# Kernel optimization log

Measured on AMD Instinct MI355X. Metric: run time of the kernel, lower is better.

Reference implementation:

```python
import jax, jax.numpy as jnp
import numpy as np

MAX_CH = 21
LAT_DIM = 64
D_EMBED = 1024
N_HEADS = 16
D_HEAD = D_EMBED // N_HEADS  # 64
L = MAX_CH * LAT_DIM         # 1344 latents
B, T = 4, 1024


def setup_inputs() -> dict:
    key = jax.random.key(0)
    k1, k2, k3, k4, k5, k6 = jax.random.split(key, 6)
    x = jax.random.normal(k1, (B, T, D_EMBED), dtype=jnp.float32)
    # boolean channel mask [b, L, T]
    ch_mask = jax.random.randint(k2, (B, L, T), 0, 2) > 0
    # learned latent queries [L, H*d] (xavier-uniform-ish init)
    lim_q = float(np.sqrt(6.0 / (L + N_HEADS * D_HEAD)))
    latent_q = jax.random.uniform(k3, (L, N_HEADS * D_HEAD), minval=-lim_q, maxval=lim_q, dtype=jnp.float32)
    # Linear weights (torch layout: [out, in]) and biases
    lim_w = float(np.sqrt(1.0 / D_EMBED))
    w_k_w = jax.random.uniform(k4, (N_HEADS * D_HEAD, D_EMBED), minval=-lim_w, maxval=lim_w, dtype=jnp.float32)
    w_k_b = jnp.zeros((N_HEADS * D_HEAD,), dtype=jnp.float32)
    w_v_w = jax.random.uniform(k5, (N_HEADS * D_HEAD, D_EMBED), minval=-lim_w, maxval=lim_w, dtype=jnp.float32)
    w_v_b = jax.random.uniform(k6, (N_HEADS * D_HEAD,), minval=-lim_w, maxval=lim_w, dtype=jnp.float32)
    return {"x": x, "ch_mask": ch_mask, "latent_q": latent_q,
            "w_k_w": w_k_w, "w_k_b": w_k_b, "w_v_w": w_v_w, "w_v_b": w_v_b}


def reference(x, ch_mask, latent_q, w_k_w, w_k_b, w_v_w, w_v_b):
    b, t, d = x.shape
    H, dh = N_HEADS, D_HEAD
    l = latent_q.shape[0]
    # faithful to torch .view(-1, H, L, d): raw row-major reinterpretation
    lq = latent_q.reshape(1, H, l, dh)                    # [1,H,L,dh]
    k = (x @ w_k_w.T + w_k_b).reshape(b, t, H, dh).transpose(0, 2, 3, 1)  # [b,H,dh,T]
    v = (x @ w_v_w.T + w_v_b).reshape(b, t, H, dh).transpose(0, 2, 1, 3)  # [b,H,T,dh]
    scale = jnp.float32(H) ** -0.5  # note: n_heads**-0.5, as in source
    scores = jnp.einsum('ohld,bhdt->bhlt', lq, k) * scale  # [b,H,L,T]
    mask = ch_mask[:, None, :, :]                           # [b,1,L,T] broadcast over heads
    scores = jnp.where(mask, scores, jnp.float32(-1e9))
    w = jax.nn.softmax(scores, axis=-1)
    w = jnp.where(mask, w, jnp.float32(0.0))
    out = jnp.einsum('bhlt,bhtd->bhld', w, v)               # [b,H,L,dh]
    return out.transpose(0, 2, 1, 3).reshape(b, l, H * dh)  # [b,L,H*dh]
```

## Files before the change

kernel.cpp:

```cpp
#include <hip/hip_runtime.h>
#include <hip/hip_bf16.h>

#define B_SZ 4
#define T_SZ 1024
#define NH 16
#define L_SZ 1344
#define LT_COUNT 21

typedef __attribute__((ext_vector_type(8))) short short8;
typedef __attribute__((ext_vector_type(4))) short short4v;
typedef __attribute__((ext_vector_type(4))) float floatx4;

typedef __attribute__((address_space(1))) const void gvoid;
typedef __attribute__((address_space(3))) void svoid;
#define GLD16(gp, lp) \
  __builtin_amdgcn_global_load_lds((gvoid*)(gp), (svoid*)(lp), 16, 0, 0)

static __device__ inline short bf16bits(float f) {
  return __builtin_bit_cast(short, __float2bfloat16(f));
}
static __device__ inline short4v cvt4(float4 v) {
  short4v r;
  r.x = bf16bits(v.x); r.y = bf16bits(v.y);
  r.z = bf16bits(v.z); r.w = bf16bits(v.w);
  return r;
}

static __device__ inline unsigned pack_bf16_2(float a, float b) {
  unsigned ua = __builtin_bit_cast(unsigned, a) + 0x8000u;
  unsigned ub = __builtin_bit_cast(unsigned, b) + 0x8000u;
  return __builtin_amdgcn_perm(ub, ua, 0x07060302u);
}
static __device__ inline uint2 pack_bf16_4(float4 v) {
  return make_uint2(pack_bf16_2(v.x, v.y), pack_bf16_2(v.z, v.w));
}


__global__ __launch_bounds__(256) void mask_detect(
    const unsigned char* __restrict__ m, int* __restrict__ flag) {
  __shared__ int any_off4, any_at4;
  if (threadIdx.x == 0) { any_off4 = 0; any_at4 = 0; }
  __syncthreads();
  int a1 = 0, a2 = 0;
  for (int i = threadIdx.x; i < 4096; i += 256) {
    unsigned char v = m[i];
    if (v) {
      if ((i & 3) != 0) a1 = 1;
      if ((i & 7) == 4) a2 = 1;
    }
  }
  if (a1) atomicOr(&any_off4, 1);
  if (a2) atomicOr(&any_at4, 1);
  __syncthreads();
  if (threadIdx.x == 0) *flag = any_off4 ? 1 : (any_at4 ? 0 : 2);
}

__global__ __launch_bounds__(256) void maskbits_kernel(
    const void* __restrict__ mask, const int* __restrict__ flag,
    unsigned int* __restrict__ bits) {
  int idx = blockIdx.x * 256 + threadIdx.x;
  int f = *flag;
  bool v;
  if (f == 1)      v = ((const signed char*)mask)[idx] != 0;
  else if (f == 2) v = ((const long long*)mask)[idx] != 0;
  else             v = ((const int*)mask)[idx] != 0;
  unsigned long long bal = __ballot(v);
  int lane = threadIdx.x & 63;
  if ((lane & 31) == 0) {
    unsigned int w = (lane & 32) ? (unsigned int)(bal >> 32) : (unsigned int)bal;
    bits[idx >> 5] = w;
  }
}

__global__ __launch_bounds__(256) void cvt_bf16(
    const float4* __restrict__ src, uint2* __restrict__ dst) {
  size_t i = (size_t)blockIdx.x * 256 + threadIdx.x;
  dst[i] = pack_bf16_4(src[i]);
}

static __device__ __forceinline__ void epi_k(const floatx4 acc[4][4],
    int bxt, int byd, int wm, int wn, int c15, int kq,
    const float* __restrict__ bk, __hip_bfloat16* __restrict__ k_buf) {
  #pragma unroll
  for (int ni = 0; ni < 4; ++ni) {
    int gr = bxt * 128 + wn * 64 + ni * 16 + c15;
    int b = gr >> 10, tc = (gr >> 6) & 15;
    #pragma unroll
    for (int mi = 0; mi < 4; ++mi) {
      int d0 = byd * 128 + wm * 64 + mi * 16 + kq * 4;
      int h = d0 >> 6, hd = d0 & 63;
      int half = hd >> 5, q4 = (hd >> 3) & 3, jlo = hd & 7;
      int bh = b * 16 + h;
      float4 b4 = *(const float4*)(bk + d0);
      float4 v4 = {acc[mi][ni][0] + b4.x, acc[mi][ni][1] + b4.y,
                   acc[mi][ni][2] + b4.z, acc[mi][ni][3] + b4.w};
      *(uint2*)(k_buf + ((size_t)((bh * 16 + tc) * 8 + ni * 2 + half)) * 512 +
                (q4 * 16 + c15) * 8 + jlo) = pack_bf16_4(v4);
    }
  }
}

static __device__ __forceinline__ void epi_v(const floatx4 acc[4][4],
    int bxd, int byt, int wm, int wn, int c15, int kq,
    const float* __restrict__ bv, __hip_bfloat16* __restrict__ v_buf) {
  #pragma unroll
  for (int ni = 0; ni < 4; ++ni) {
    int d = bxd * 128 + wn * 64 + ni * 16 + c15;
    int h = d >> 6;
    float bias = bv[d];
    #pragma unroll
    for (int mi = 0; mi < 4; ++mi) {
      int gr = byt * 128 + wm * 64 + mi * 16 + kq * 4;
      int b = gr >> 10, tc = (gr >> 6) & 15;
      int tl = gr & 63;
      int half = tl >> 5, q4 = (tl >> 3) & 3, jlo = tl & 7;
      int bh = b * 16 + h;
      float4 v4 = {acc[mi][ni][0] + bias, acc[mi][ni][1] + bias,
                   acc[mi][ni][2] + bias, acc[mi][ni][3] + bias};
      *(uint2*)(v_buf + ((size_t)((bh * 16 + tc) * 8 + ni * 2 + half)) * 512 +
                (q4 * 16 + c15) * 8 + jlo) = pack_bf16_4(v4);
    }
  }
}

static __device__ __forceinline__ void gemm_core(
    const __hip_bfloat16* __restrict__ A, const __hip_bfloat16* __restrict__ B,
    __hip_bfloat16* ldsA, __hip_bfloat16* ldsB,
    int TA, int TB, int tid, floatx4 (&acc)[4][4]) {
  const int lane = tid & 63, w = tid >> 6;
  const int wm = w & 1, wn = w >> 1;
  const int c15 = lane & 15, kq = lane >> 4;
  for (int kk = 0; kk < 1024; kk += 32) {
    #pragma unroll
    for (int j = 0; j < 2; ++j) {
      int c = w * 128 + j * 64 + lane;
      int row = c >> 2;
      int gkc = (c & 3) ^ (row & 3);
      GLD16(A + (size_t)(TA * 128 + row) * 1024 + kk + gkc * 8,
            ldsA + (w * 128 + j * 64) * 8);
      GLD16(B + (size_t)(TB * 128 + row) * 1024 + kk + gkc * 8,
            ldsB + (w * 128 + j * 64) * 8);
    }
    __syncthreads();
    short8 af[4], bf[4];
    #pragma unroll
    for (int mi = 0; mi < 4; ++mi) {
      int row = wm * 64 + mi * 16 + c15;
      af[mi] = *(const short8*)(ldsA + row * 32 + ((kq ^ (row & 3)) * 8));
    }
    #pragma unroll
    for (int ni = 0; ni < 4; ++ni) {
      int row = wn * 64 + ni * 16 + c15;
      bf[ni] = *(const short8*)(ldsB + row * 32 + ((kq ^ (row & 3)) * 8));
    }
    #pragma unroll
    for (int mi = 0; mi < 4; ++mi)
      #pragma unroll
      for (int ni = 0; ni < 4; ++ni)
        acc[mi][ni] = __builtin_amdgcn_mfma_f32_16x16x32_bf16(
            af[mi], bf[ni], acc[mi][ni], 0, 0, 0);
    __syncthreads();
  }
}

__global__ __launch_bounds__(256) void gemm_kv_bf16(
    const __hip_bfloat16* __restrict__ xb,
    const __hip_bfloat16* __restrict__ wkb, const __hip_bfloat16* __restrict__ wvb,
    const float* __restrict__ bk, const float* __restrict__ bv,
    __hip_bfloat16* __restrict__ k_buf, __hip_bfloat16* __restrict__ v_buf) {
  __shared__ __align__(16) __hip_bfloat16 ldsA[128 * 32];
  __shared__ __align__(16) __hip_bfloat16 ldsB[128 * 32];
  const int tid = threadIdx.x;
  const int lane = tid & 63, w = tid >> 6;
  const int wm = w & 1, wn = w >> 1;
  const int c15 = lane & 15, kq = lane >> 4;
  floatx4 acc[4][4];
  for (int i = 0; i < 4; ++i)
    for (int j = 0; j < 4; ++j) acc[i][j] = (floatx4){0.f, 0.f, 0.f, 0.f};

  if (blockIdx.z == 0) {
    gemm_core(wkb, xb, ldsA, ldsB, blockIdx.y, blockIdx.x, tid, acc);
    epi_k(acc, blockIdx.x, blockIdx.y, wm, wn, c15, kq, bk, k_buf);
  } else {
    gemm_core(xb, wvb, ldsA, ldsB, blockIdx.x, blockIdx.y, tid, acc);
    epi_v(acc, blockIdx.y, blockIdx.x, wm, wn, c15, kq, bv, v_buf);
  }
}

__global__ __launch_bounds__(256, 3) void attn_kernel(
    const float* __restrict__ latent_q,
    const __hip_bfloat16* __restrict__ k_buf,
    const __hip_bfloat16* __restrict__ v_buf,
    const unsigned int* __restrict__ mbits,
    float* __restrict__ out) {
  __shared__ __align__(16) __hip_bfloat16 pbuf[4][16 * 72];
  __shared__ uint2 mrows[64][17];

  const int tid = threadIdx.x;
  const int lane = tid & 63;
  const int w = tid >> 6;
  int bid = blockIdx.x;
  int xcd = bid & 7, j = bid >> 3;
  int bh = xcd * 8 + j / LT_COUNT;
  int lt = j % LT_COUNT;
  int h = bh & 15, b = bh >> 4;
  const int q4 = lane >> 4, c15 = lane & 15;
  const int l0 = lt * 64;

  {
    const unsigned int* msrc = mbits + (size_t)(b * L_SZ + l0) * 32;
    #pragma unroll
    for (int p = 0; p < 2; ++p) {
      int i = p * 256 + tid;
      uint4 m4 = *(const uint4*)(msrc + i * 4);
      int row = i >> 3, c2 = (i & 7) * 2;
      mrows[row][c2]     = make_uint2(m4.x, m4.y);
      mrows[row][c2 + 1] = make_uint2(m4.z, m4.w);
    }
  }
  __syncthreads();

  const float QS = 0.25f * 1.44269504089f;
  short8 qf[2];
  {
    const float* qp = latent_q + ((size_t)(h * L_SZ + l0 + w * 16 + c15)) * 64 + q4 * 8;
    float4 a0 = *(const float4*)(qp);
    float4 a1 = *(const float4*)(qp + 4);
    float4 a2 = *(const float4*)(qp + 32);
    float4 a3 = *(const float4*)(qp + 36);
    a0.x *= QS; a0.y *= QS; a0.z *= QS; a0.w *= QS;
    a1.x *= QS; a1.y *= QS; a1.z *= QS; a1.w *= QS;
    a2.x *= QS; a2.y *= QS; a2.z *= QS; a2.w *= QS;
    a3.x *= QS; a3.y *= QS; a3.z *= QS; a3.w *= QS;
    short4v t0 = cvt4(a0), t1 = cvt4(a1), t2 = cvt4(a2), t3 = cvt4(a3);
    qf[0] = (short8){t0.x, t0.y, t0.z, t0.w, t1.x, t1.y, t1.z, t1.w};
    qf[1] = (short8){t2.x, t2.y, t2.z, t2.w, t3.x, t3.y, t3.z, t3.w};
  }

  floatx4 l4 = (floatx4){0.f, 0.f, 0.f, 0.f};
  floatx4 o_acc[4];
  #pragma unroll
  for (int di = 0; di < 4; ++di) o_acc[di] = (floatx4){0.f, 0.f, 0.f, 0.f};

  const __hip_bfloat16* kb = k_buf + (size_t)bh * 65536;
  const __hip_bfloat16* vb = v_buf + (size_t)bh * 65536;
  __hip_bfloat16* pw = pbuf[w];

  for (int tc = 0; tc < 16; ++tc) {
    short8 kf[2][4], vf[2][4];
    #pragma unroll
    for (int half = 0; half < 2; ++half)
      #pragma unroll
      for (int ni = 0; ni < 4; ++ni)
        kf[half][ni] = *(const short8*)(kb + (size_t)(tc * 8 + ni * 2 + half) * 512 + lane * 8);
    #pragma unroll
    for (int half = 0; half < 2; ++half)
      #pragma unroll
      for (int di = 0; di < 4; ++di)
        vf[half][di] = *(const short8*)(vb + (size_t)(tc * 8 + di * 2 + half) * 512 + lane * 8);

    uint2 mw = mrows[w * 16 + c15][tc];
    floatx4 s[4];
    #pragma unroll
    for (int ni = 0; ni < 4; ++ni) s[ni] = (floatx4){0.f, 0.f, 0.f, 0.f};
    #pragma unroll
    for (int half = 0; half < 2; ++half)
      #pragma unroll
      for (int ni = 0; ni < 4; ++ni)
        s[ni] = __builtin_amdgcn_mfma_f32_16x16x32_bf16(kf[half][ni], qf[half], s[ni], 0, 0, 0);
    #pragma unroll
    for (int ni = 0; ni < 4; ++ni) {
      unsigned mword = (ni >= 2) ? mw.y : mw.x;
      float4 p4;
      #pragma unroll
      for (int r = 0; r < 4; ++r) {
        float e = exp2f(s[ni][r]);
        int sh = (ni & 1) * 16 + q4 * 4 + r;
        ((float*)&p4)[r] = ((mword >> sh) & 1) ? e : 0.f;
      }
      l4[0] += p4.x; l4[1] += p4.y;
      l4[2] += p4.z; l4[3] += p4.w;
      *(uint2*)(pw + c15 * 72 + ni * 16 + q4 * 4) = pack_bf16_4(p4);
    }

    short8 pf0 = *(const short8*)(pw + c15 * 72 + q4 * 8);
    short8 pf1 = *(const short8*)(pw + c15 * 72 + 32 + q4 * 8);
    #pragma unroll
    for (int di = 0; di < 4; ++di)
      o_acc[di] = __builtin_amdgcn_mfma_f32_16x16x32_bf16(vf[0][di], pf0, o_acc[di], 0, 0, 0);
    #pragma unroll
    for (int di = 0; di < 4; ++di)
      o_acc[di] = __builtin_amdgcn_mfma_f32_16x16x32_bf16(vf[1][di], pf1, o_acc[di], 0, 0, 0);
  }

  float la = (l4[0] + l4[1]) + (l4[2] + l4[3]);
  la += __shfl_xor(la, 16, 64);
  la += __shfl_xor(la, 32, 64);
  float inv = (la > 0.f) ? 1.f / la : 0.f;
  float* ob = out + ((size_t)(b * L_SZ + l0 + w * 16 + c15)) * 1024 + h * 64;
  #pragma unroll
  for (int di = 0; di < 4; ++di) {
    float4 o4 = {o_acc[di][0] * inv, o_acc[di][1] * inv,
                 o_acc[di][2] * inv, o_acc[di][3] * inv};
    *(float4*)(ob + di * 16 + q4 * 4) = o4;
  }
}

extern "C" void kernel_launch(void* const* d_in, const int* in_sizes, int n_in,
                              void* d_out, int out_size, void* d_ws, size_t ws_size,
                              hipStream_t stream) {
  const float* x      = (const float*)d_in[0];
  const void* ch_mask = d_in[1];
  const float* lq     = (const float*)d_in[2];
  const float* wk     = (const float*)d_in[3];
  const float* bk     = (const float*)d_in[4];
  const float* wv     = (const float*)d_in[5];
  const float* bv     = (const float*)d_in[6];
  float* out = (float*)d_out;

  char* ws = (char*)d_ws;
  unsigned int* mbits   = (unsigned int*)ws;
  int* flag             = (int*)(ws + 720896);
  __hip_bfloat16* k_buf = (__hip_bfloat16*)(ws + 786432);
  __hip_bfloat16* v_buf = (__hip_bfloat16*)(ws + 786432 + 8388608);

  __hip_bfloat16* xb  = (__hip_bfloat16*)d_out;
  __hip_bfloat16* wkb = xb + 4 * 1024 * 1024;
  __hip_bfloat16* wvb = wkb + 1024 * 1024;

  mask_detect<<<1, 256, 0, stream>>>((const unsigned char*)ch_mask, flag);
  maskbits_kernel<<<21504, 256, 0, stream>>>(ch_mask, flag, mbits);

  cvt_bf16<<<4096, 256, 0, stream>>>((const float4*)x, (uint2*)xb);
  cvt_bf16<<<1024, 256, 0, stream>>>((const float4*)wk, (uint2*)wkb);
  cvt_bf16<<<1024, 256, 0, stream>>>((const float4*)wv, (uint2*)wvb);
  gemm_kv_bf16<<<dim3(32, 8, 2), 256, 0, stream>>>(xb, wkb, wvb, bk, bv, k_buf, v_buf);

  attn_kernel<<<8 * 168, 256, 0, stream>>>(lq, k_buf, v_buf, mbits, out);
}
```

Baseline: 207.7 us.

## Stage K/V tiles in LDS with double-buffered async global-to-LDS loads

Instead of each wave loading identical K and V fragments from global memory into registers, the block cooperatively copies each T-chunk of K and V into LDS via global_load_lds, double-buffered so the next chunk prefetches while the current one is computed. Waves then read fragments from LDS. This removes the fourfold redundant global traffic and hides load latency, at the cost of extra LDS usage and two barriers per iteration that may lower occupancy or add sync stalls.

```diff
diff --git a/kernel.cpp b/kernel.cpp
--- a/kernel.cpp
+++ b/kernel.cpp
@@ -193,6 +193,8 @@
     const __hip_bfloat16* __restrict__ v_buf,
     const unsigned int* __restrict__ mbits,
     float* __restrict__ out) {
+  __shared__ __align__(16) __hip_bfloat16 ldsK[2][4096];
+  __shared__ __align__(16) __hip_bfloat16 ldsV[2][4096];
   __shared__ __align__(16) __hip_bfloat16 pbuf[4][16 * 72];
   __shared__ uint2 mrows[64][17];
 
@@ -218,7 +220,6 @@
       mrows[row][c2 + 1] = make_uint2(m4.z, m4.w);
     }
   }
-  __syncthreads();
 
   const float QS = 0.25f * 1.44269504089f;
   short8 qf[2];
@@ -236,6 +237,7 @@
     qf[0] = (short8){t0.x, t0.y, t0.z, t0.w, t1.x, t1.y, t1.z, t1.w};
     qf[1] = (short8){t2.x, t2.y, t2.z, t2.w, t3.x, t3.y, t3.z, t3.w};
   }
+  __syncthreads();
 
   floatx4 l4 = (floatx4){0.f, 0.f, 0.f, 0.f};
   floatx4 o_acc[4];
@@ -246,19 +248,34 @@
   const __hip_bfloat16* vb = v_buf + (size_t)bh * 65536;
   __hip_bfloat16* pw = pbuf[w];
 
+#define STAGE_KV(sb, tcn) do {                                              \
+    const __hip_bfloat16* gk_ = kb + (size_t)(tcn) * 4096;                  \
+    const __hip_bfloat16* gv_ = vb + (size_t)(tcn) * 4096;                  \
+    int o0_ = w * 512 + lane * 8;                                           \
+    GLD16(gk_ + o0_,        &ldsK[sb][w * 512]);                            \
+    GLD16(gk_ + 2048 + o0_, &ldsK[sb][2048 + w * 512]);                     \
+    GLD16(gv_ + o0_,        &ldsV[sb][w * 512]);                            \
+    GLD16(gv_ + 2048 + o0_, &ldsV[sb][2048 + w * 512]);                     \
+  } while (0)
+
+  STAGE_KV(0, 0);
+
   for (int tc = 0; tc < 16; ++tc) {
-    short8 kf[2][4], vf[2][4];
+    const int buf = tc & 1;
+    if (tc + 1 < 16) {
+      STAGE_KV(buf ^ 1, tc + 1);
+      asm volatile("s_waitcnt vmcnt(4)" ::: "memory");
+    } else {
+      asm volatile("s_waitcnt vmcnt(0)" ::: "memory");
+    }
+    __builtin_amdgcn_s_barrier();
+
+    short8 kf[2][4];
     #pragma unroll
     for (int half = 0; half < 2; ++half)
       #pragma unroll
       for (int ni = 0; ni < 4; ++ni)
-        kf[half][ni] = *(const short8*)(kb + (size_t)(tc * 8 + ni * 2 + half) * 512 + lane * 8);
-    #pragma unroll
-    for (int half = 0; half < 2; ++half)
-      #pragma unroll
-      for (int di = 0; di < 4; ++di)
-        vf[half][di] = *(const short8*)(vb + (size_t)(tc * 8 + di * 2 + half) * 512 + lane * 8);
-
+        kf[half][ni] = *(const short8*)(&ldsK[buf][(ni * 2 + half) * 512 + lane * 8]);
     uint2 mw = mrows[w * 16 + c15][tc];
     floatx4 s[4];
     #pragma unroll
@@ -268,6 +285,14 @@
       #pragma unroll
       for (int ni = 0; ni < 4; ++ni)
         s[ni] = __builtin_amdgcn_mfma_f32_16x16x32_bf16(kf[half][ni], qf[half], s[ni], 0, 0, 0);
+
+    short8 vf[2][4];
+    #pragma unroll
+    for (int half = 0; half < 2; ++half)
+      #pragma unroll
+      for (int di = 0; di < 4; ++di)
+        vf[half][di] = *(const short8*)(&ldsV[buf][(di * 2 + half) * 512 + lane * 8]);
+
     #pragma unroll
     for (int ni = 0; ni < 4; ++ni) {
       unsigned mword = (ni >= 2) ? mw.y : mw.x;
@@ -291,7 +316,11 @@
     #pragma unroll
     for (int di = 0; di < 4; ++di)
       o_acc[di] = __builtin_amdgcn_mfma_f32_16x16x32_bf16(vf[1][di], pf1, o_acc[di], 0, 0, 0);
-  }
+
+    asm volatile("s_waitcnt lgkmcnt(0)" ::: "memory");
+    __builtin_amdgcn_s_barrier();
+  }
+#undef STAGE_KV
 
   float la = (l4[0] + l4[1]) + (l4[2] + l4[3]);
   la += __shfl_xor(la, 16, 64);
```

Measured after the change: 199.4 us. 1.04x faster.
